# Performance work log

Hardware: AMD Instinct MI355X
Metric: run time of the kernel (lower is better)

Reference implementation:

```python
import jax, jax.numpy as jnp
import numpy as np
import math

# Hardware quantization constants (Parameter.* in the original repo)
IP = 8        # Parameter.InputPrecesion
ADCP = 5      # Parameter.ADCPrecision
IE = 1        # Parameter.InputEncoding
ADCMAX = 8.0  # Parameter.ADCMax
K = 3         # kernel_size
STRIDE = 1
PAD = 1


def _quant(x, level, vmax):
    # torch: sep = linspace(0, Max, level); x = sep[searchsorted(sep, x + sep[1]/2) - 1]
    # i.e. round-to-nearest onto a uniform grid, saturating at vmax.
    sep = jnp.linspace(0.0, vmax, level, dtype=x.dtype)
    idx = jnp.searchsorted(sep, x + sep[1] * 0.5) - 1
    return jnp.take(sep, idx, mode='clip')


def _conv(x, w):
    return jax.lax.conv_general_dilated(
        x, w, window_strides=(STRIDE, STRIDE),
        padding=[(PAD, PAD), (PAD, PAD)],
        dimension_numbers=('NCHW', 'OIHW', 'NCHW'))


def setup_inputs() -> dict:
    key = jax.random.key(0)
    kx, kw = jax.random.split(key)
    x = jax.random.uniform(kx, (32, 256, 56, 56), dtype=jnp.float32)  # post-ReLU-like, >= 0
    weight = jax.random.normal(kw, (256, 256, 3, 3), dtype=jnp.float32) * 0.01
    return {"x": x, "weight": weight}


def reference(x, weight):
    # split weight into positive / negative conductance arrays
    pweight = jnp.maximum(weight, 0.0)
    nweight = jnp.maximum(-weight, 0.0)
    # input DAC quantization (input.min() >= 0 branch)
    xq = _quant(x, 2 ** IP, ADCMAX)
    # two convs (quant_dev_back is identity in forward), then ADC requant
    lvl_out = K * K * 2 ** (ADCP + math.ceil(IP / IE))
    outpos = _quant(_conv(xq, pweight), lvl_out, ADCMAX)
    outneg = _quant(_conv(xq, nweight), lvl_out, ADCMAX)
    return outpos - outneg
```

## Files before the change

### kernel.cpp

```cpp
#include <hip/hip_runtime.h>

typedef int int32x4 __attribute__((ext_vector_type(4)));

#define B_ 32
#define C_ 256
#define H_ 56
#define W_ 56

static constexpr float QSCALE = 255.0f / 8.0f;
static constexpr float D1 = 8.0f / 255.0f;

#define PLANE 53824
#define BSTR  861184
static constexpr size_t XQ_BYTES = (size_t)B_ * BSTR;
static constexpr size_t XQ_SPACE = XQ_BYTES + 32768;
static constexpr size_t WT_SPACE = 38ull * 16384;
static constexpr size_t WS_NEED = XQ_SPACE + WT_SPACE + 2048;

#define XROWB 3744
#define XBUFB (4 * XROWB)

__device__ __forceinline__ void gload_lds16(const void* g, void* l) {
  __builtin_amdgcn_global_load_lds((const __attribute__((address_space(1))) unsigned int*)g,
                                   (__attribute__((address_space(3))) unsigned int*)l,
                                   16, 0, 0);
}

__global__ __launch_bounds__(256) void quant_transpose_i8(const float* __restrict__ x,
                                                          char* __restrict__ Xq) {
  __shared__ __align__(16) char T8[58 * 272];
  const int h = blockIdx.x;
  const int b = blockIdx.y;
  const int tid = threadIdx.x;
  const int c = tid;

  T8[0 * 272 + c] = 0;
  T8[57 * 272 + c] = 0;

  const float4* src = (const float4*)(x + (((size_t)b * C_ + c) * H_ + h) * W_);
#pragma unroll
  for (int i = 0; i < 14; ++i) {
    float4 v = src[i];
    float vals[4] = {v.x, v.y, v.z, v.w};
    const int w0 = i * 4;
#pragma unroll
    for (int j = 0; j < 4; ++j) {
      int n = (int)rintf(vals[j] * QSCALE);
      n = n < 0 ? 0 : (n > 255 ? 255 : n);
      T8[(w0 + j + 1) * 272 + c] = (char)n;
    }
  }
  __syncthreads();

  char* Xb = Xq + (size_t)b * BSTR;
#pragma unroll
  for (int p = 0; p < 4; ++p) {
    if (tid < 232) {
      const int w = tid % 58;
      const int cig = p * 4 + tid / 58;
      *(int4*)(Xb + (size_t)cig * PLANE + (h + 1) * 928 + w * 16) =
          *(const int4*)&T8[w * 272 + cig * 16];
    }
  }

  if (h == 0 || h == 55) {
    const int hb = (h == 0) ? 0 : 57;
    const int4 z = {0, 0, 0, 0};
    for (int i = tid; i < 928; i += 256) {
      const int w = i % 58;
      const int cig = i / 58;
      *(int4*)(Xb + (size_t)cig * PLANE + hb * 928 + w * 16) = z;
    }
  }
}

__global__ __launch_bounds__(256) void prep_weights_i8(const float* __restrict__ w,
                                                       char* __restrict__ Wt,
                                                       float* __restrict__ oscale) {
  __shared__ __align__(16) float wf[2304];
  __shared__ __align__(16) char Wq[2304];
  __shared__ float red[4];
  __shared__ float sbc;
  const int co = blockIdx.x;
  const int tid = threadIdx.x;

  const float4* src = (const float4*)(w + (size_t)co * 2304);
  float m = 0.f;
  for (int i = tid; i < 576; i += 256) {
    float4 v = src[i];
    *(float4*)&wf[i * 4] = v;
    m = fmaxf(fmaxf(fabsf(v.x), fabsf(v.y)), fmaxf(fmaxf(fabsf(v.z), fabsf(v.w)), m));
  }

#pragma unroll
  for (int off = 32; off; off >>= 1) m = fmaxf(m, __shfl_down(m, off));
  if ((tid & 63) == 0) red[tid >> 6] = m;
  __syncthreads();
  if (tid == 0) {
    m = fmaxf(fmaxf(red[0], red[1]), fmaxf(red[2], red[3]));
    m = fmaxf(m, 1e-20f);
    sbc = m;
    oscale[co] = (m / 127.f) * D1;
  }
  __syncthreads();

  if (tid < 9) {
    const int p = tid;
    const float s = sbc / 127.f;
    const float inv = 1.f / s;
    float carry = 0.f;
    for (int ci = 0; ci < 256; ++ci) {
      float t = wf[ci * 9 + p] + carry;
      float qf = rintf(t * inv);
      qf = fminf(fmaxf(qf, -128.f), 127.f);
      carry = t - qf * s;
      Wq[((ci >> 6) * 9 + p) * 64 + (ci & 63)] = (char)(int)qf;
    }
  }
  __syncthreads();

  if (tid < 144) {
    const int chunk = tid >> 2;
    const int g = tid & 3;
    int4 v = *(const int4*)&Wq[chunk * 64 + (g << 4)];
    *(int4*)(Wt + ((size_t)(chunk * 256 + co)) * 64 + (g << 4)) = v;
  }
}

__global__ __launch_bounds__(256, 4) void conv_mfma_i8(const char* __restrict__ Xq,
                                                       const char* __restrict__ Wt,
                                                       const float* __restrict__ oscale,
                                                       float* __restrict__ out) {
  __shared__ __align__(16) char Xl[XBUFB];
  const int tid = threadIdx.x;
  const int wid = tid >> 6, lane = tid & 63;
  const int col = lane & 15, hi = lane >> 4;

  const int l = blockIdx.x;
  const int wk = (l & 7) * 224 + (l >> 3);
  const int mh = wk & 1;
  const int rest = wk >> 1;
  const int by = rest % 28;
  const int b = rest / 28;
  const int h0 = 2 * by;

  int banf[7];
#pragma unroll
  for (int nf = 0; nf < 7; ++nf) {
    const int n_out = nf * 16 + col;
    const int r = n_out >= 56 ? 1 : 0;
    banf[nf] = hi * XROWB + (r * 58 + (n_out - r * 56)) * 16;
  }

  int32x4 acc[2][7];
#pragma unroll
  for (int mf = 0; mf < 2; ++mf)
#pragma unroll
    for (int nf = 0; nf < 7; ++nf) acc[mf][nf] = (int32x4){0, 0, 0, 0};

  const char* Xqb = Xq + (size_t)b * BSTR + h0 * 928;
  const char* wg = Wt + (size_t)((mh * 128 + wid * 32 + col) * 64 + hi * 16);

  int32x4 Wc0, Wc1, Wn0, Wn1;

#pragma unroll
  for (int q = 0; q < 4; ++q)
    if (tid < 232) gload_lds16(Xqb + (size_t)q * PLANE + tid * 16,
                               Xl + q * XROWB + tid * 16);
  Wc0 = *(const int32x4*)(wg);
  Wc1 = *(const int32x4*)(wg + 1024);
  Wn0 = *(const int32x4*)(wg + 16384);
  Wn1 = *(const int32x4*)(wg + 16384 + 1024);
  __syncthreads();

#define MSTEP(POS, PROW16)                                                               \
  {                                                                                      \
    __builtin_amdgcn_s_setprio(1);                                                       \
    _Pragma("unroll") for (int nf = 0; nf < 7; ++nf) {                                   \
      int32x4 bb = *(const int32x4*)(Xl + banf[nf] + (PROW16));                          \
      acc[0][nf] = __builtin_amdgcn_mfma_i32_16x16x64_i8(Wc0, bb, acc[0][nf], 0, 0, 0);  \
      acc[1][nf] = __builtin_amdgcn_mfma_i32_16x16x64_i8(Wc1, bb, acc[1][nf], 0, 0, 0);  \
    }                                                                                    \
    __builtin_amdgcn_s_setprio(0);                                                       \
    Wc0 = Wn0; Wc1 = Wn1;                                                                \
    Wn0 = *(const int32x4*)(wgcc + ((POS) + 2) * 16384);                                 \
    Wn1 = *(const int32x4*)(wgcc + ((POS) + 2) * 16384 + 1024);                          \
  }

  const char* wgcc = wg;
#pragma unroll 1
  for (int cc = 0; cc < 4; ++cc) {
    MSTEP(0, 0)
    MSTEP(1, 16)
    MSTEP(2, 32)
    MSTEP(3, 928)
    MSTEP(4, 944)
    MSTEP(5, 960)
    MSTEP(6, 1856)
    MSTEP(7, 1872)
    MSTEP(8, 1888)
    if (cc < 3) {
      __syncthreads();
      const char* xsrc = Xqb + (size_t)(4 * (cc + 1)) * PLANE;
#pragma unroll
      for (int q = 0; q < 4; ++q)
        if (tid < 232) gload_lds16(xsrc + (size_t)q * PLANE + tid * 16,
                                   Xl + q * XROWB + tid * 16);
      __syncthreads();
    }
    wgcc += 9 * 16384;
  }
#undef MSTEP

#pragma unroll
  for (int mf = 0; mf < 2; ++mf) {
    const int cbase = mh * 128 + wid * 32 + mf * 16 + hi * 4;
    const float4 os = *(const float4*)(oscale + cbase);
#pragma unroll
    for (int nf = 0; nf < 7; ++nf) {
      const int n_out = nf * 16 + col;
      const int r = n_out >= 56 ? 1 : 0;
      const int hrow = h0 + r;
      const int wcol = n_out - r * 56;
      float* o = out + ((((size_t)b * 256 + cbase) * 56 + hrow) * 56 + wcol);
      o[0 * 3136] = (float)acc[mf][nf][0] * os.x;
      o[1 * 3136] = (float)acc[mf][nf][1] * os.y;
      o[2 * 3136] = (float)acc[mf][nf][2] * os.z;
      o[3 * 3136] = (float)acc[mf][nf][3] * os.w;
    }
  }
}

__global__ void conv_naive(const float* __restrict__ x, const float* __restrict__ w,
                           float* __restrict__ out, int total) {
  int idx = blockIdx.x * 256 + threadIdx.x;
  if (idx >= total) return;
  const int wc = idx % 56;
  int t = idx / 56;
  const int hr = t % 56; t /= 56;
  const int co = t % 256;
  const int b = t / 256;
  float acc = 0.f;
  for (int ci = 0; ci < 256; ++ci) {
    const float* xb = x + (((size_t)b * 256 + ci) * 56) * 56;
    const float* wb = w + ((size_t)co * 256 + ci) * 9;
#pragma unroll
    for (int kh = 0; kh < 3; ++kh) {
      const int hh = hr + kh - 1;
      if (hh < 0 || hh >= 56) continue;
#pragma unroll
      for (int kw = 0; kw < 3; ++kw) {
        const int ww = wc + kw - 1;
        if (ww < 0 || ww >= 56) continue;
        const float q = rintf(xb[hh * 56 + ww] * QSCALE) * D1;
        acc += q * wb[kh * 3 + kw];
      }
    }
  }
  out[idx] = acc;
}

extern "C" void kernel_launch(void* const* d_in, const int* in_sizes, int n_in,
                              void* d_out, int out_size, void* d_ws, size_t ws_size,
                              hipStream_t stream) {
  (void)in_sizes; (void)n_in; (void)out_size;
  const float* x = (const float*)d_in[0];
  const float* w = (const float*)d_in[1];
  float* out = (float*)d_out;

  if (ws_size < WS_NEED) {
    const int total = B_ * C_ * H_ * W_;
    conv_naive<<<(total + 255) / 256, 256, 0, stream>>>(x, w, out, total);
    return;
  }

  char* Xq = (char*)d_ws;
  char* Wt = (char*)d_ws + XQ_SPACE;
  float* oscale = (float*)((char*)d_ws + XQ_SPACE + WT_SPACE);

  quant_transpose_i8<<<dim3(56, 32), 256, 0, stream>>>(x, Xq);
  prep_weights_i8<<<dim3(256), 256, 0, stream>>>(w, Wt, oscale);
  conv_mfma_i8<<<dim3(1792), 256, 0, stream>>>(Xq, Wt, oscale, out);
}
```

Measured before the change: 94.65 us.

## Switch int8 conv to 32x32x32 MFMA with double-buffered LDS and new tiling

Replaces the 16x16x64 int8 MFMA tiling (2 output rows × 128 channels per block) with 32x32x32 MFMA tiles covering all 256 output channels over 64 flattened pixels per block. The input and weight layouts move to 32-channel groups, and the LDS input buffer is double-buffered, with the next channel group's loads issued between MFMA steps. The goal is to remove the two barriers per chunk and the load stall, and to get more reuse per LDS read from the larger MFMA. The cost is 8 K-iterations instead of 4, fewer blocks, and a different output store pattern.

```diff
diff --git a/kernel.cpp b/kernel.cpp
--- a/kernel.cpp
+++ b/kernel.cpp
@@ -1,6 +1,7 @@
 #include <hip/hip_runtime.h>
 
 typedef int int32x4 __attribute__((ext_vector_type(4)));
+typedef int int32x16 __attribute__((ext_vector_type(16)));
 
 #define B_ 32
 #define C_ 256
@@ -10,15 +11,15 @@
 static constexpr float QSCALE = 255.0f / 8.0f;
 static constexpr float D1 = 8.0f / 255.0f;
 
-#define PLANE 53824
+#define PLANE 107648
 #define BSTR  861184
 static constexpr size_t XQ_BYTES = (size_t)B_ * BSTR;
 static constexpr size_t XQ_SPACE = XQ_BYTES + 32768;
-static constexpr size_t WT_SPACE = 38ull * 16384;
+static constexpr size_t WT_SPACE = 74ull * 8192;
 static constexpr size_t WS_NEED = XQ_SPACE + WT_SPACE + 2048;
 
-#define XROWB 3744
-#define XBUFB (4 * XROWB)
+#define XROWH 3728
+#define XBUF  7456
 
 __device__ __forceinline__ void gload_lds16(const void* g, void* l) {
   __builtin_amdgcn_global_load_lds((const __attribute__((address_space(1))) unsigned int*)g,
@@ -56,10 +57,13 @@
 #pragma unroll
   for (int p = 0; p < 4; ++p) {
     if (tid < 232) {
-      const int w = tid % 58;
-      const int cig = p * 4 + tid / 58;
-      *(int4*)(Xb + (size_t)cig * PLANE + (h + 1) * 928 + w * 16) =
-          *(const int4*)&T8[w * 272 + cig * 16];
+      const int idx = p * 232 + tid;
+      const int cig = idx / 116;
+      const int rem = idx % 116;
+      const int w = rem >> 1;
+      const int g = rem & 1;
+      *(int4*)(Xb + (size_t)cig * PLANE + (h + 1) * 1856 + w * 32 + g * 16) =
+          *(const int4*)&T8[w * 272 + cig * 32 + g * 16];
     }
   }
 
@@ -67,9 +71,9 @@
     const int hb = (h == 0) ? 0 : 57;
     const int4 z = {0, 0, 0, 0};
     for (int i = tid; i < 928; i += 256) {
-      const int w = i % 58;
-      const int cig = i / 58;
-      *(int4*)(Xb + (size_t)cig * PLANE + hb * 928 + w * 16) = z;
+      const int cig = i / 116;
+      const int rem = i % 116;
+      *(int4*)(Xb + (size_t)cig * PLANE + hb * 1856 + (rem >> 1) * 32 + (rem & 1) * 16) = z;
     }
   }
 }
@@ -114,16 +118,16 @@
       float qf = rintf(t * inv);
       qf = fminf(fmaxf(qf, -128.f), 127.f);
       carry = t - qf * s;
-      Wq[((ci >> 6) * 9 + p) * 64 + (ci & 63)] = (char)(int)qf;
+      Wq[((ci >> 5) * 9 + p) * 32 + (ci & 31)] = (char)(int)qf;
     }
   }
   __syncthreads();
 
   if (tid < 144) {
-    const int chunk = tid >> 2;
-    const int g = tid & 3;
-    int4 v = *(const int4*)&Wq[chunk * 64 + (g << 4)];
-    *(int4*)(Wt + ((size_t)(chunk * 256 + co)) * 64 + (g << 4)) = v;
+    const int kstep = tid >> 1;
+    const int g = tid & 1;
+    int4 v = *(const int4*)&Wq[kstep * 32 + (g << 4)];
+    *(int4*)(Wt + ((size_t)(kstep * 256 + co)) * 32 + (g << 4)) = v;
   }
 }
 
@@ -131,66 +135,70 @@
                                                        const char* __restrict__ Wt,
                                                        const float* __restrict__ oscale,
                                                        float* __restrict__ out) {
-  __shared__ __align__(16) char Xl[XBUFB];
+  __shared__ __align__(16) char Xl[2][XBUF];
   const int tid = threadIdx.x;
   const int wid = tid >> 6, lane = tid & 63;
-  const int col = lane & 15, hi = lane >> 4;
+  const int c31 = lane & 31, h2 = lane >> 5;
 
   const int l = blockIdx.x;
-  const int wk = (l & 7) * 224 + (l >> 3);
-  const int mh = wk & 1;
-  const int rest = wk >> 1;
-  const int by = rest % 28;
-  const int b = rest / 28;
-  const int h0 = 2 * by;
-
-  int banf[7];
-#pragma unroll
-  for (int nf = 0; nf < 7; ++nf) {
-    const int n_out = nf * 16 + col;
-    const int r = n_out >= 56 ? 1 : 0;
-    banf[nf] = hi * XROWB + (r * 58 + (n_out - r * 56)) * 16;
-  }
-
-  int32x4 acc[2][7];
-#pragma unroll
-  for (int mf = 0; mf < 2; ++mf)
-#pragma unroll
-    for (int nf = 0; nf < 7; ++nf) acc[mf][nf] = (int32x4){0, 0, 0, 0};
-
-  const char* Xqb = Xq + (size_t)b * BSTR + h0 * 928;
-  const char* wg = Wt + (size_t)((mh * 128 + wid * 32 + col) * 64 + hi * 16);
+  const int wk = (l & 7) * 196 + (l >> 3);
+  const int b = wk / 49;
+  const int sb = wk % 49;
+  const int n0 = sb * 64;
+  const int rlo = n0 / 56;
+
+  int banf[2];
+#pragma unroll
+  for (int nf = 0; nf < 2; ++nf) {
+    const int n = n0 + nf * 32 + c31;
+    const int r = n / 56;
+    const int w = n - r * 56;
+    banf[nf] = h2 * XROWH + ((r - rlo) * 58 + w) * 16;
+  }
+
+  int32x16 c00 = {0}, c01 = {0}, c10 = {0}, c11 = {0};
+
+  const char* xqb = Xq + (size_t)b * BSTR + rlo * 1856;
+  const char* wg = Wt + (size_t)((wid * 64 + c31) * 32) + h2 * 16;
 
   int32x4 Wc0, Wc1, Wn0, Wn1;
 
-#pragma unroll
-  for (int q = 0; q < 4; ++q)
-    if (tid < 232) gload_lds16(Xqb + (size_t)q * PLANE + tid * 16,
-                               Xl + q * XROWB + tid * 16);
+  if (tid < 232) {
+    gload_lds16(xqb + tid * 32, (char*)Xl + tid * 16);
+    gload_lds16(xqb + tid * 32 + 16, (char*)Xl + XROWH + tid * 16);
+  }
   Wc0 = *(const int32x4*)(wg);
   Wc1 = *(const int32x4*)(wg + 1024);
-  Wn0 = *(const int32x4*)(wg + 16384);
-  Wn1 = *(const int32x4*)(wg + 16384 + 1024);
-  __syncthreads();
-
-#define MSTEP(POS, PROW16)                                                               \
-  {                                                                                      \
-    __builtin_amdgcn_s_setprio(1);                                                       \
-    _Pragma("unroll") for (int nf = 0; nf < 7; ++nf) {                                   \
-      int32x4 bb = *(const int32x4*)(Xl + banf[nf] + (PROW16));                          \
-      acc[0][nf] = __builtin_amdgcn_mfma_i32_16x16x64_i8(Wc0, bb, acc[0][nf], 0, 0, 0);  \
-      acc[1][nf] = __builtin_amdgcn_mfma_i32_16x16x64_i8(Wc1, bb, acc[1][nf], 0, 0, 0);  \
-    }                                                                                    \
-    __builtin_amdgcn_s_setprio(0);                                                       \
-    Wc0 = Wn0; Wc1 = Wn1;                                                                \
-    Wn0 = *(const int32x4*)(wgcc + ((POS) + 2) * 16384);                                 \
-    Wn1 = *(const int32x4*)(wgcc + ((POS) + 2) * 16384 + 1024);                          \
+  Wn0 = *(const int32x4*)(wg + 8192);
+  Wn1 = *(const int32x4*)(wg + 8192 + 1024);
+  __syncthreads();
+
+#define MSTEP(POS, PROW16)                                                                \
+  {                                                                                       \
+    int32x4 b0 = *(const int32x4*)(xl + banf[0] + (PROW16));                              \
+    int32x4 b1 = *(const int32x4*)(xl + banf[1] + (PROW16));                              \
+    __builtin_amdgcn_s_setprio(1);                                                        \
+    c00 = __builtin_amdgcn_mfma_i32_32x32x32_i8(Wc0, b0, c00, 0, 0, 0);                   \
+    c01 = __builtin_amdgcn_mfma_i32_32x32x32_i8(Wc0, b1, c01, 0, 0, 0);                   \
+    c10 = __builtin_amdgcn_mfma_i32_32x32x32_i8(Wc1, b0, c10, 0, 0, 0);                   \
+    c11 = __builtin_amdgcn_mfma_i32_32x32x32_i8(Wc1, b1, c11, 0, 0, 0);                   \
+    __builtin_amdgcn_s_setprio(0);                                                        \
+    Wc0 = Wn0; Wc1 = Wn1;                                                                 \
+    Wn0 = *(const int32x4*)(wgcc + ((POS) + 2) * 8192);                                   \
+    Wn1 = *(const int32x4*)(wgcc + ((POS) + 2) * 8192 + 1024);                            \
   }
 
   const char* wgcc = wg;
 #pragma unroll 1
-  for (int cc = 0; cc < 4; ++cc) {
+  for (int cc8 = 0; cc8 < 8; ++cc8) {
+    const char* xl = (const char*)Xl + (cc8 & 1) * XBUF;
+    char* xnxt = (char*)Xl + ((cc8 & 1) ^ 1) * XBUF;
+    const char* xsrc = xqb + (size_t)(cc8 + 1) * PLANE;
+    const bool st = (cc8 < 7);
+
+    if (st && tid < 232) gload_lds16(xsrc + tid * 32, xnxt + tid * 16);
     MSTEP(0, 0)
+    if (st && tid < 232) gload_lds16(xsrc + tid * 32 + 16, xnxt + XROWH + tid * 16);
     MSTEP(1, 16)
     MSTEP(2, 32)
     MSTEP(3, 928)
@@ -199,34 +207,28 @@
     MSTEP(6, 1856)
     MSTEP(7, 1872)
     MSTEP(8, 1888)
-    if (cc < 3) {
-      __syncthreads();
-      const char* xsrc = Xqb + (size_t)(4 * (cc + 1)) * PLANE;
-#pragma unroll
-      for (int q = 0; q < 4; ++q)
-        if (tid < 232) gload_lds16(xsrc + (size_t)q * PLANE + tid * 16,
-                                   Xl + q * XROWB + tid * 16);
-      __syncthreads();
-    }
-    wgcc += 9 * 16384;
+    if (st) __syncthreads();
+    wgcc += 9 * 8192;
   }
 #undef MSTEP
 
 #pragma unroll
-  for (int mf = 0; mf < 2; ++mf) {
-    const int cbase = mh * 128 + wid * 32 + mf * 16 + hi * 4;
-    const float4 os = *(const float4*)(oscale + cbase);
-#pragma unroll
-    for (int nf = 0; nf < 7; ++nf) {
-      const int n_out = nf * 16 + col;
-      const int r = n_out >= 56 ? 1 : 0;
-      const int hrow = h0 + r;
-      const int wcol = n_out - r * 56;
-      float* o = out + ((((size_t)b * 256 + cbase) * 56 + hrow) * 56 + wcol);
-      o[0 * 3136] = (float)acc[mf][nf][0] * os.x;
-      o[1 * 3136] = (float)acc[mf][nf][1] * os.y;
-      o[2 * 3136] = (float)acc[mf][nf][2] * os.z;
-      o[3 * 3136] = (float)acc[mf][nf][3] * os.w;
+  for (int mfrag = 0; mfrag < 2; ++mfrag) {
+    const int cob2 = wid * 64 + mfrag * 32 + 4 * h2;
+    const float4 o0 = *(const float4*)(oscale + cob2);
+    const float4 o1 = *(const float4*)(oscale + cob2 + 8);
+    const float4 o2 = *(const float4*)(oscale + cob2 + 16);
+    const float4 o3 = *(const float4*)(oscale + cob2 + 24);
+    const float osv[16] = {o0.x, o0.y, o0.z, o0.w, o1.x, o1.y, o1.z, o1.w,
+                           o2.x, o2.y, o2.z, o2.w, o3.x, o3.y, o3.z, o3.w};
+#pragma unroll
+    for (int nf = 0; nf < 2; ++nf) {
+      const int n = n0 + nf * 32 + c31;
+      float* o = out + (size_t)(b * 256 + cob2) * 3136 + n;
+      const int32x16 cc = mfrag == 0 ? (nf == 0 ? c00 : c01) : (nf == 0 ? c10 : c11);
+#pragma unroll
+      for (int r = 0; r < 16; ++r)
+        o[(size_t)((r & 3) + 8 * (r >> 2)) * 3136] = (float)cc[r] * osv[r];
     }
   }
 }
@@ -280,5 +282,5 @@
 
   quant_transpose_i8<<<dim3(56, 32), 256, 0, stream>>>(x, Xq);
   prep_weights_i8<<<dim3(256), 256, 0, stream>>>(w, Wt, oscale);
-  conv_mfma_i8<<<dim3(1792), 256, 0, stream>>>(Xq, Wt, oscale, out);
-}
+  conv_mfma_i8<<<dim3(1568), 256, 0, stream>>>(Xq, Wt, oscale, out);
+}
```

Result: slower. 109.1 us (+15.3%).
